# Kernel optimization log

Measured on AMD Instinct MI355X. Metric: run time of the kernel, lower is better.

Reference implementation:

```python
import jax, jax.numpy as jnp
import numpy as np

HIDDEN = 768
NUM_HEADS = 12
HEAD_DIM = HIDDEN // NUM_HEADS
WINDOW = 128
NEG = -1e30  # stand-in for -inf that is safe under autodiff


def setup_inputs() -> dict:
    key = jax.random.key(0)
    ks = jax.random.split(key, 12)
    B, S = 2, 2048
    hidden = jax.random.normal(ks[0], (B, S, HIDDEN), dtype=jnp.float32)
    attention_mask = jnp.ones((B, S), dtype=jnp.int32)
    global_mask = jax.random.randint(ks[1], (B, S), 0, 2, dtype=jnp.int32)
    def lin(kw, kb):
        W = jax.random.normal(kw, (HIDDEN, HIDDEN), dtype=jnp.float32) * 0.02
        b = jax.random.normal(kb, (HIDDEN,), dtype=jnp.float32) * 0.02
        return W, b
    Wq, bq = lin(ks[2], ks[3])
    Wk, bk = lin(ks[4], ks[5])
    Wv, bv = lin(ks[6], ks[7])
    Wo, bo = lin(ks[8], ks[9])
    return {"hidden": hidden, "attention_mask": attention_mask, "global_mask": global_mask,
            "Wq": Wq, "bq": bq, "Wk": Wk, "bk": bk, "Wv": Wv, "bv": bv, "Wo": Wo, "bo": bo}


def _attend(hidden, attention_mask, global_mask, Wq, bq, Wk, bk, Wv, bv, Wo, bo):
    B, S, H = hidden.shape
    def proj(W, b):
        # (B,S,H) -> (B,nh,S,hd); nn.Linear computes x @ W.T + b
        return (hidden @ W.T + b).reshape(B, S, NUM_HEADS, HEAD_DIM).transpose(0, 2, 1, 3)
    q, k, v = proj(Wq, bq), proj(Wk, bk), proj(Wv, bv)
    scale = jnp.asarray(np.sqrt(HEAD_DIM), dtype=hidden.dtype)
    scores = jnp.einsum('bhqd,bhkd->bhqk', q, k) / scale  # (B,nh,S,S)
    # sliding window mask: |i-j| <= WINDOW
    idx = jnp.arange(S)
    window = (jnp.abs(idx[:, None] - idx[None, :]) <= WINDOW)  # (S,S)
    g = global_mask.astype(bool)
    combined = window[None] | g[:, :, None] | g[:, None, :]     # (B,S,S)
    combined = combined & attention_mask.astype(bool)[:, None, :]  # pad mask on keys
    scores = jnp.where(combined[:, None, :, :], scores, NEG)
    attn = jax.nn.softmax(scores, axis=-1)
    # torch code zeroes NaN rows (fully masked); replicate safely
    attn = jnp.where(jnp.isnan(attn), 0.0, attn)
    out = jnp.einsum('bhqk,bhkd->bhqd', attn, v)  # (B,nh,S,hd)
    out = out.transpose(0, 2, 1, 3).reshape(B, S, H)
    return out @ Wo.T + bo


def reference(hidden, attention_mask, global_mask, Wq, bq, Wk, bk, Wv, bv, Wo, bo):
    return _attend(hidden, attention_mask, global_mask, Wq, bq, Wk, bk, Wv, bv, Wo, bo)
```

## Files before the change

### kernel.cpp

```cpp
#include <hip/hip_runtime.h>
#include <math.h>

#define S_LEN 2048
#define HID   768
#define NH    12
#define HD    64
#define WIN   128
#define NEGV  (-1e30f)
#define QSCALE 0.1803368801111204f

typedef __attribute__((ext_vector_type(8))) short short8v;
typedef __attribute__((ext_vector_type(4))) float float4v;
typedef unsigned short u16;

__device__ __forceinline__ u16 f2bf(float f) {
    union { float f; unsigned int u; } c; c.f = f;
    unsigned int u = c.u + 0x7FFFu + ((c.u >> 16) & 1u);
    return (u16)(u >> 16);
}

__device__ __forceinline__ short8v cvt8(float4 a, float4 b) {
    short8v t;
    t[0]=(short)f2bf(a.x); t[1]=(short)f2bf(a.y); t[2]=(short)f2bf(a.z); t[3]=(short)f2bf(a.w);
    t[4]=(short)f2bf(b.x); t[5]=(short)f2bf(b.y); t[6]=(short)f2bf(b.z); t[7]=(short)f2bf(b.w);
    return t;
}

__device__ __forceinline__ unsigned int pk2bf(float a, float b) {
    unsigned int r;
    asm("v_cvt_pk_bf16_f32 %0, %1, %2" : "=v"(r) : "v"(a), "v"(b));
    return r;
}

__device__ __forceinline__ float exp2_fast(float x) {
    float r;
    asm("v_exp_f32 %0, %1" : "=v"(r) : "v"(x));
    return r;
}

__device__ __forceinline__ void gload_lds16(const void* g, void* l) {
    __builtin_amdgcn_global_load_lds(
        (const __attribute__((address_space(1))) unsigned int*)g,
        (__attribute__((address_space(3))) unsigned int*)l, 16, 0, 0);
}

__global__ __launch_bounds__(256) void convert_inputs(
    const float* __restrict__ hidden, const float* __restrict__ Wq,
    const float* __restrict__ Wk, const float* __restrict__ Wv,
    const float* __restrict__ Wo, u16* __restrict__ hbf, u16* __restrict__ w4)
{
    const int y = blockIdx.y;
    const float* src; u16* dst; int n; float scale = 1.f;
    if (y == 0) { src = hidden; dst = hbf; n = 4096*HID; }
    else {
        src = (y==1) ? Wq : (y==2) ? Wk : (y==3) ? Wv : Wo;
        dst = w4 + (size_t)(y-1)*HID*HID;
        n = HID*HID;
        if (y == 1) scale = QSCALE;
    }
    const int idx = (blockIdx.x*256 + threadIdx.x) * 8;
    if (idx >= n) return;
    float4 f0 = *(const float4*)(src + idx);
    float4 f1 = *(const float4*)(src + idx + 4);
    f0.x*=scale; f0.y*=scale; f0.z*=scale; f0.w*=scale;
    f1.x*=scale; f1.y*=scale; f1.z*=scale; f1.w*=scale;
    *(short8v*)(dst + idx) = cvt8(f0, f1);
}

__global__ __launch_bounds__(256) void gemm_mfma(
    const u16* __restrict__ A, const u16* __restrict__ W4,
    const float* __restrict__ bA, const float* __restrict__ bB,
    const float* __restrict__ bC, u16* __restrict__ obf,
    u16* __restrict__ ovt, float* __restrict__ of32, int mode)
{
    __shared__ __align__(16) u16 As[128*32];
    __shared__ __align__(16) u16 Bs[128*32];

    const int tid = threadIdx.x;
    const int w = tid >> 6, l = tid & 63;
    const int lx = l & 15, lg = l >> 4;
    const int wr = w >> 1, wc = w & 1;
    const int m0 = blockIdx.x * 128, n0 = blockIdx.y * 128;
    const int z = (mode == 0) ? blockIdx.z : 3;
    const float* bias = (mode == 1) ? bA : (z == 0 ? bA : (z == 1 ? bB : bC));
    const float bscale = (mode == 0 && z == 0) ? QSCALE : 1.0f;
    const u16* Wp = W4 + (size_t)z * (HID*HID);

    float4v acc[4][4];
    const float4v fz = {0.f,0.f,0.f,0.f};
    #pragma unroll
    for (int i = 0; i < 4; i++)
        #pragma unroll
        for (int j = 0; j < 4; j++) acc[i][j] = fz;

    for (int kt = 0; kt < HID/32; kt++) {
        const int k0 = kt * 32;
        __syncthreads();
        #pragma unroll
        for (int rnd = 0; rnd < 2; rnd++) {
            const int ch  = rnd*256 + w*64 + l;
            const int row = ch >> 2, kc = ch & 3;
            gload_lds16(A  + (size_t)(m0+row)*HID + k0 + kc*8,
                        As + (size_t)(rnd*256 + w*64)*8);
            gload_lds16(Wp + (size_t)(n0+row)*HID + k0 + kc*8,
                        Bs + (size_t)(rnd*256 + w*64)*8);
        }
        __syncthreads();
        short8v af[4], bfr[4];
        #pragma unroll
        for (int i = 0; i < 4; i++) {
            af[i]  = *(const short8v*)(As + (wr*64 + i*16 + lx)*32 + lg*8);
            bfr[i] = *(const short8v*)(Bs + (wc*64 + i*16 + lx)*32 + lg*8);
        }
        #pragma unroll
        for (int i = 0; i < 4; i++)
            #pragma unroll
            for (int j = 0; j < 4; j++)
                acc[i][j] = __builtin_amdgcn_mfma_f32_16x16x32_bf16(af[i], bfr[j], acc[i][j], 0, 0, 0);
    }

    #pragma unroll
    for (int j = 0; j < 4; j++) {
        const int col = n0 + wc*64 + j*16 + lx;
        const float bval = bias[col] * bscale;
        const int hh = col >> 6, d = col & 63;
        #pragma unroll
        for (int i = 0; i < 4; i++) {
            const int rbase = m0 + wr*64 + i*16 + lg*4;
            const int bb = rbase >> 11, s = rbase & 2047;
            const float v0 = acc[i][j][0] + bval;
            const float v1 = acc[i][j][1] + bval;
            const float v2 = acc[i][j][2] + bval;
            const float v3 = acc[i][j][3] + bval;
            if (mode == 1) {
                of32[(size_t)(rbase+0)*HID + col] = v0;
                of32[(size_t)(rbase+1)*HID + col] = v1;
                of32[(size_t)(rbase+2)*HID + col] = v2;
                of32[(size_t)(rbase+3)*HID + col] = v3;
            } else if (z == 2) {
                uint2 ow; ow.x = pk2bf(v0, v1); ow.y = pk2bf(v2, v3);
                *(uint2*)&ovt[(((size_t)bb*NH + hh)*HD + d)*S_LEN + s] = ow;
            } else {
                u16* base = obf + (size_t)z * ((size_t)2*S_LEN*HID);
                base[(((size_t)bb*NH + hh)*S_LEN + s+0)*HD + d] = f2bf(v0);
                base[(((size_t)bb*NH + hh)*S_LEN + s+1)*HD + d] = f2bf(v1);
                base[(((size_t)bb*NH + hh)*S_LEN + s+2)*HD + d] = f2bf(v2);
                base[(((size_t)bb*NH + hh)*S_LEN + s+3)*HD + d] = f2bf(v3);
            }
        }
    }
}

__global__ __launch_bounds__(256) void attn_mfma(
    const u16* __restrict__ Q, const u16* __restrict__ K,
    const u16* __restrict__ Vt, const int* __restrict__ amask,
    const int* __restrict__ gmask, u16* __restrict__ AO)
{
    __shared__ __align__(16) u16 KsA[64*64], VsA[64*64];
    __shared__ __align__(16) u16 KsB[64*64], VsB[64*64];
    __shared__ __align__(16) u16 Ps[4*16*64];
    __shared__ __align__(16) float fAa[64], fBa[64];
    __shared__ __align__(16) float fAb[64], fBb[64];

    const int tid = threadIdx.x;
    const int w  = tid >> 6;
    const int l  = tid & 63;
    const int lx = l & 15;
    const int lg = l >> 4;

    const int bid = blockIdx.x;
    const int swz = (bid & 7) * 96 + (bid >> 3);
    const int q0 = (swz & 31) * 64;
    const int hb = swz >> 5;
    const int h  = hb % NH;
    const int b  = hb / NH;
    const size_t bh = ((size_t)b*NH + h) * S_LEN;

    const int q_glob = q0 + w*16 + lx;

    short8v aq[2];
    {
        const u16* qp = Q + (bh + q_glob)*HD + lg*8;
        aq[0] = *(const short8v*)(qp);
        aq[1] = *(const short8v*)(qp + 32);
    }
    const int gq = gmask[(size_t)b*S_LEN + q_glob];
    const float* fPa = gq ? fAa : fBa;
    const float* fPb = gq ? fAb : fBb;

    float m_i = NEGV, l_i = 0.f;
    float4v o_acc[4];
    const float4v fzv = {0.f, 0.f, 0.f, 0.f};
    #pragma unroll
    for (int db = 0; db < 4; db++) o_acc[db] = fzv;

    const int str = tid >> 2;
    const int stc = tid & 3;
    const int rb  = str * 128;
    const int sw  = (str & 7) << 4;
    const u16* Kbase = K + bh * HD;
    const u16* Vbase = Vt + (size_t)(b*NH + h) * HD * S_LEN;
    const int psw = (lx & 7) << 4;

    uint4 rk0, rk1, rv0, rv1;
    int ram = 0, rgk = 0;

#define STAGE_REGS(KT) do {                                                   \
    const int kk0_ = (KT) * 64;                                               \
    const u16* kp_ = Kbase + (size_t)(kk0_ + str)*HD + stc*16;                \
    rk0 = *(const uint4*)(kp_); rk1 = *(const uint4*)(kp_ + 8);               \
    const u16* vp_ = Vbase + (size_t)str*S_LEN + kk0_ + stc*16;               \
    rv0 = *(const uint4*)(vp_); rv1 = *(const uint4*)(vp_ + 8);               \
    if (tid < 64) {                                                           \
        ram = amask[(size_t)b*S_LEN + kk0_ + tid];                            \
        rgk = gmask[(size_t)b*S_LEN + kk0_ + tid];                            \
    }                                                                         \
} while(0)

#define WRITE_LDS(KS, VS, FA, FB) do {                                        \
    *(uint4*)((char*)(KS) + rb + ((stc*32)      ^ sw)) = rk0;                 \
    *(uint4*)((char*)(KS) + rb + ((stc*32 + 16) ^ sw)) = rk1;                 \
    *(uint4*)((char*)(VS) + rb + ((stc*32)      ^ sw)) = rv0;                 \
    *(uint4*)((char*)(VS) + rb + ((stc*32 + 16) ^ sw)) = rv1;                 \
    if (tid < 64) {                                                           \
        (FA)[tid] = ram ? 0.f : NEGV;                                         \
        (FB)[tid] = (ram && rgk) ? 0.f : NEGV;                                \
    }                                                                         \
} while(0)

#define COMPUTE(KS, VS, FA, FB, FP, K0) do {                                  \
                           \
    float4v sacc[4];                                                          \
    const int adq_ = ((K0) > q0) ? ((K0) - q0) : (q0 - (K0));                 \
    if (adq_ <= 64) {                                                         \
        _Pragma("unroll")                                                     \
        for (int kb = 0; kb < 4; kb++) {                                      \
            float4 fa4 = *(const float4*)&(FA)[kb*16 + lg*4];                 \
            sacc[kb][0]=fa4.x; sacc[kb][1]=fa4.y;                             \
            sacc[kb][2]=fa4.z; sacc[kb][3]=fa4.w;                             \
        }                                                                     \
    } else if (adq_ >= 192) {                                                 \
        _Pragma("unroll")                                                     \
        for (int kb = 0; kb < 4; kb++) {                                      \
            float4 fp4 = *(const float4*)&(FP)[kb*16 + lg*4];                 \
            sacc[kb][0]=fp4.x; sacc[kb][1]=fp4.y;                             \
            sacc[kb][2]=fp4.z; sacc[kb][3]=fp4.w;                             \
        }                                                                     \
    } else {                                                                  \
        _Pragma("unroll")                                                     \
        for (int kb = 0; kb < 4; kb++) {                                      \
            float4 fa4 = *(const float4*)&(FA)[kb*16 + lg*4];                 \
            float4 fb4 = *(const float4*)&(FB)[kb*16 + lg*4];                 \
            const int e_ = q_glob - ((K0) + kb*16 + lg*4);                    \
            _Pragma("unroll")                                                 \
            for (int r = 0; r < 4; r++) {                                     \
                int dd_ = e_ - r; dd_ = dd_ < 0 ? -dd_ : dd_;                 \
                const bool wing_ = (dd_ <= WIN) || gq;                        \
                sacc[kb][r] = wing_ ? (&fa4.x)[r] : (&fb4.x)[r];              \
            }                                                                 \
        }                                                                     \
    }                                                                         \
    __builtin_amdgcn_s_setprio(1);                                            \
    _Pragma("unroll")                                                         \
    for (int kb = 0; kb < 4; kb++) {                                          \
        const int key_ = kb*16 + lx;                                          \
        const int ksw_ = (key_ & 7) << 4;                                     \
        _Pragma("unroll")                                                     \
        for (int ks = 0; ks < 2; ks++) {                                      \
            short8v bk_ = *(const short8v*)((char*)(KS) + key_*128 +          \
                                            ((16*lg + 64*ks) ^ ksw_));        \
            sacc[kb] = __builtin_amdgcn_mfma_f32_16x16x32_bf16(bk_, aq[ks],   \
                                                          sacc[kb], 0, 0, 0); \
        }                                                                     \
    }                                                                         \
    __builtin_amdgcn_s_setprio(0);                                            \
                                \
    float mloc;                                                               \
    {                                                                         \
        float t0 = fmaxf(fmaxf(sacc[0][0], sacc[0][1]), sacc[0][2]);          \
        float t1 = fmaxf(fmaxf(sacc[0][3], sacc[1][0]), sacc[1][1]);          \
        float t2 = fmaxf(fmaxf(sacc[1][2], sacc[1][3]), sacc[2][0]);          \
        float t3 = fmaxf(fmaxf(sacc[2][1], sacc[2][2]), sacc[2][3]);          \
        float t4 = fmaxf(fmaxf(sacc[3][0], sacc[3][1]), sacc[3][2]);          \
        mloc = fmaxf(fmaxf(fmaxf(t0, t1), t2),                                \
                     fmaxf(fmaxf(t3, t4), sacc[3][3]));                       \
    }                                                                         \
    mloc = fmaxf(mloc, __shfl_xor(mloc, 16));                                 \
    mloc = fmaxf(mloc, __shfl_xor(mloc, 32));                                 \
    if (__any(mloc > m_i + 8.0f)) {                                           \
        const float mnew_ = fmaxf(m_i, mloc);                                 \
        const float sc_ = exp2_fast(m_i - mnew_);                             \
        l_i *= sc_;                                                           \
        _Pragma("unroll")                                                     \
        for (int db = 0; db < 4; db++)                                        \
            _Pragma("unroll")                                                 \
            for (int r = 0; r < 4; r++) o_acc[db][r] *= sc_;                  \
        m_i = mnew_;                                                          \
    }                                                                         \
    float p[4][4];                                                            \
    _Pragma("unroll")                                                         \
    for (int kb = 0; kb < 4; kb++)                                            \
        _Pragma("unroll")                                                     \
        for (int r = 0; r < 4; r++)                                           \
            p[kb][r] = exp2_fast(sacc[kb][r] - m_i);                          \
    {                                                                         \
        float s0 = (p[0][0]+p[0][1]) + (p[0][2]+p[0][3]);                     \
        float s1 = (p[1][0]+p[1][1]) + (p[1][2]+p[1][3]);                     \
        float s2 = (p[2][0]+p[2][1]) + (p[2][2]+p[2][3]);                     \
        float s3 = (p[3][0]+p[3][1]) + (p[3][2]+p[3][3]);                     \
        float lsum = (s0+s1) + (s2+s3);                                       \
        lsum += __shfl_xor(lsum, 16);                                         \
        lsum += __shfl_xor(lsum, 32);                                         \
        l_i += lsum;                                                          \
    }                                                                         \
    _Pragma("unroll")                                                         \
    for (int kb = 0; kb < 4; kb++) {                                          \
        uint2 pw;                                                             \
        pw.x = pk2bf(p[kb][0], p[kb][1]);                                     \
        pw.y = pk2bf(p[kb][2], p[kb][3]);                                     \
        *(uint2*)((char*)Ps + w*2048 + lx*128 + ((kb*32 + lg*8) ^ psw)) = pw; \
    }                                                                         \
    __builtin_amdgcn_s_setprio(1);                                            \
    _Pragma("unroll")                                                         \
    for (int ks = 0; ks < 2; ks++) {                                          \
        short8v pa_ = *(const short8v*)((char*)Ps + w*2048 + lx*128 +         \
                                        ((16*lg + 64*ks) ^ psw));             \
        _Pragma("unroll")                                                     \
        for (int db = 0; db < 4; db++) {                                      \
            const int drow_ = db*16 + lx;                                     \
            short8v bv_ = *(const short8v*)((char*)(VS) + drow_*128 +         \
                                    ((16*lg + 64*ks) ^ ((drow_ & 7) << 4)));  \
            o_acc[db] = __builtin_amdgcn_mfma_f32_16x16x32_bf16(bv_, pa_,     \
                                                          o_acc[db], 0, 0, 0);\
        }                                                                     \
    }                                                                         \
    __builtin_amdgcn_s_setprio(0);                                            \
} while(0)

    STAGE_REGS(0);
    WRITE_LDS(KsA, VsA, fAa, fBa);
    __syncthreads();

    for (int kt = 0; kt < S_LEN/64; kt += 2) {
        STAGE_REGS(kt+1);
        COMPUTE(KsA, VsA, fAa, fBa, fPa, kt*64);
        WRITE_LDS(KsB, VsB, fAb, fBb);
        __syncthreads();
        {
            const int kn = (kt+2 < S_LEN/64) ? (kt+2) : (S_LEN/64 - 1);
            STAGE_REGS(kn);
        }
        COMPUTE(KsB, VsB, fAb, fBb, fPb, (kt+1)*64);
        WRITE_LDS(KsA, VsA, fAa, fBa);
        __syncthreads();
    }

#undef STAGE_REGS
#undef WRITE_LDS
#undef COMPUTE

    {
        const float inv = 1.f / l_i;
        u16* op = AO + ((size_t)b*S_LEN + q_glob)*HID + h*HD + lg*4;
        #pragma unroll
        for (int db = 0; db < 4; db++) {
            uint2 ow;
            ow.x = pk2bf(o_acc[db][0]*inv, o_acc[db][1]*inv);
            ow.y = pk2bf(o_acc[db][2]*inv, o_acc[db][3]*inv);
            *(uint2*)(op + db*16) = ow;
        }
    }
}

extern "C" void kernel_launch(void* const* d_in, const int* in_sizes, int n_in,
                              void* d_out, int out_size, void* d_ws, size_t ws_size,
                              hipStream_t stream)
{
    const float* hidden = (const float*)d_in[0];
    const int*   amask  = (const int*)d_in[1];
    const int*   gmask  = (const int*)d_in[2];
    const float* Wq = (const float*)d_in[3];
    const float* bq = (const float*)d_in[4];
    const float* Wk = (const float*)d_in[5];
    const float* bk = (const float*)d_in[6];
    const float* Wv = (const float*)d_in[7];
    const float* bv = (const float*)d_in[8];
    const float* Wo = (const float*)d_in[9];
    const float* bo = (const float*)d_in[10];
    float* out = (float*)d_out;

    char* ws = (char*)d_ws;
    const size_t NTOK = (size_t)2 * S_LEN * HID;
    u16* hbf   = (u16*)(ws);
    u16* w4    = (u16*)(ws + 6291456);
    u16* qkvbf = (u16*)(ws + 11010048);
    u16* vtbf  = (u16*)(ws + 29884416);
    u16* aobf  = (u16*)(ws + 36175872);

    convert_inputs<<<dim3(1536, 5), 256, 0, stream>>>(hidden, Wq, Wk, Wv, Wo, hbf, w4);

    gemm_mfma<<<dim3(32, 6, 3), 256, 0, stream>>>(hbf, w4, bq, bk, bv, qkvbf, vtbf, nullptr, 0);

    u16* Qbf = qkvbf;
    u16* Kbf = qkvbf + NTOK;

    attn_mfma<<<dim3(768), 256, 0, stream>>>(Qbf, Kbf, vtbf, amask, gmask, aobf);

    gemm_mfma<<<dim3(32, 6), 256, 0, stream>>>(aobf, w4, bo, nullptr, nullptr, nullptr, nullptr, out, 1);
}
```

Measured before the change: 106.1 us.

## Split attention keys across two blocks and merge partial softmax results

The attention kernel now processes each query tile in two blocks, each covering half of the key range. Each block writes an unnormalized partial output plus its running max and sum, and a new merge kernel combines the two halves. This doubles the grid to raise occupancy and parallelism. K rows are permuted when staged into shared memory so the P fragment can be fed to the PV MFMA straight from registers, which removes the Ps LDS round-trip. The cost is an extra kernel launch and extra global traffic for the partials, plus losing the double-buffered K/V staging (now single buffer with two barriers per tile). Workspace regions that are no longer live (hidden bf16, the Wq part of the weights, Vt) are reused for the partials and the merged output.

```diff
diff --git a/kernel.cpp b/kernel.cpp
--- a/kernel.cpp
+++ b/kernel.cpp
@@ -8,6 +8,7 @@
 #define WIN   128
 #define NEGV  (-1e30f)
 #define QSCALE 0.1803368801111204f
+#define NROW  49152
 
 typedef __attribute__((ext_vector_type(8))) short short8v;
 typedef __attribute__((ext_vector_type(4))) float float4v;
@@ -36,6 +37,15 @@
     float r;
     asm("v_exp_f32 %0, %1" : "=v"(r) : "v"(x));
     return r;
+}
+
+__device__ __forceinline__ short8v mk8(unsigned a, unsigned b, unsigned c, unsigned d) {
+    union { short8v v; unsigned u[4]; } t;
+    t.u[0]=a; t.u[1]=b; t.u[2]=c; t.u[3]=d; return t.v;
+}
+
+__device__ __forceinline__ float bf2f(u16 v) {
+    union { float f; unsigned u; } c; c.u = ((unsigned)v) << 16; return c.f;
 }
 
 __device__ __forceinline__ void gload_lds16(const void* g, void* l) {
@@ -151,16 +161,16 @@
     }
 }
 
-__global__ __launch_bounds__(256) void attn_mfma(
+__global__ __launch_bounds__(256) void attn_split(
     const u16* __restrict__ Q, const u16* __restrict__ K,
     const u16* __restrict__ Vt, const int* __restrict__ amask,
-    const int* __restrict__ gmask, u16* __restrict__ AO)
+    const int* __restrict__ gmask, u16* __restrict__ O0,
+    u16* __restrict__ O1, float* __restrict__ Mp, float* __restrict__ Lp)
 {
-    __shared__ __align__(16) u16 KsA[64*64], VsA[64*64];
-    __shared__ __align__(16) u16 KsB[64*64], VsB[64*64];
-    __shared__ __align__(16) u16 Ps[4*16*64];
-    __shared__ __align__(16) float fAa[64], fBa[64];
-    __shared__ __align__(16) float fAb[64], fBb[64];
+    __shared__ __align__(16) u16 Ks[64*64];
+    __shared__ __align__(16) u16 Vs[64*64];
+    __shared__ __align__(16) float fA[64];
+    __shared__ __align__(16) float fB[64];
 
     const int tid = threadIdx.x;
     const int w  = tid >> 6;
@@ -169,9 +179,10 @@
     const int lg = l >> 4;
 
     const int bid = blockIdx.x;
-    const int swz = (bid & 7) * 96 + (bid >> 3);
-    const int q0 = (swz & 31) * 64;
-    const int hb = swz >> 5;
+    const int swz = (bid & 7) * 192 + (bid >> 3);
+    const int half = swz & 1;
+    const int q0 = ((swz >> 1) & 31) * 64;
+    const int hb = swz >> 6;
     const int h  = hb % NH;
     const int b  = hb / NH;
     const size_t bh = ((size_t)b*NH + h) * S_LEN;
@@ -185,8 +196,7 @@
         aq[1] = *(const short8v*)(qp + 32);
     }
     const int gq = gmask[(size_t)b*S_LEN + q_glob];
-    const float* fPa = gq ? fAa : fBa;
-    const float* fPb = gq ? fAb : fBb;
+    const float* fP = gq ? fA : fB;
 
     float m_i = NEGV, l_i = 0.f;
     float4v o_acc[4];
@@ -196,11 +206,14 @@
 
     const int str = tid >> 2;
     const int stc = tid & 3;
-    const int rb  = str * 128;
-    const int sw  = (str & 7) << 4;
+    const int xr  = (str & 32) | (((str>>2)&1)<<4) | (((str>>4)&1)<<3)
+                  | (((str>>3)&1)<<2) | (str & 3);
+    const int rbK = xr * 128;
+    const int swK = (xr & 7) << 4;
+    const int rbV = str * 128;
+    const int swV = (str & 7) << 4;
     const u16* Kbase = K + bh * HD;
     const u16* Vbase = Vt + (size_t)(b*NH + h) * HD * S_LEN;
-    const int psw = (lx & 7) << 4;
 
     uint4 rk0, rk1, rv0, rv1;
     int ram = 0, rgk = 0;
@@ -217,41 +230,44 @@
     }                                                                         \
 } while(0)
 
-#define WRITE_LDS(KS, VS, FA, FB) do {                                        \
-    *(uint4*)((char*)(KS) + rb + ((stc*32)      ^ sw)) = rk0;                 \
-    *(uint4*)((char*)(KS) + rb + ((stc*32 + 16) ^ sw)) = rk1;                 \
-    *(uint4*)((char*)(VS) + rb + ((stc*32)      ^ sw)) = rv0;                 \
-    *(uint4*)((char*)(VS) + rb + ((stc*32 + 16) ^ sw)) = rv1;                 \
+#define WRITE_LDS() do {                                                      \
+    *(uint4*)((char*)Ks + rbK + ((stc*32)      ^ swK)) = rk0;                 \
+    *(uint4*)((char*)Ks + rbK + ((stc*32 + 16) ^ swK)) = rk1;                 \
+    *(uint4*)((char*)Vs + rbV + ((stc*32)      ^ swV)) = rv0;                 \
+    *(uint4*)((char*)Vs + rbV + ((stc*32 + 16) ^ swV)) = rv1;                 \
     if (tid < 64) {                                                           \
-        (FA)[tid] = ram ? 0.f : NEGV;                                         \
-        (FB)[tid] = (ram && rgk) ? 0.f : NEGV;                                \
+        fA[tid] = ram ? 0.f : NEGV;                                           \
+        fB[tid] = (ram && rgk) ? 0.f : NEGV;                                  \
     }                                                                         \
 } while(0)
 
-#define COMPUTE(KS, VS, FA, FB, FP, K0) do {                                  \
-                           \
+#define COMPUTE(K0) do {                                                      \
+       \
     float4v sacc[4];                                                          \
     const int adq_ = ((K0) > q0) ? ((K0) - q0) : (q0 - (K0));                 \
     if (adq_ <= 64) {                                                         \
         _Pragma("unroll")                                                     \
         for (int kb = 0; kb < 4; kb++) {                                      \
-            float4 fa4 = *(const float4*)&(FA)[kb*16 + lg*4];                 \
+            const int base_ = 32*(kb>>1) + 8*lg + 4*(kb&1);                   \
+            float4 fa4 = *(const float4*)&fA[base_];                          \
             sacc[kb][0]=fa4.x; sacc[kb][1]=fa4.y;                             \
             sacc[kb][2]=fa4.z; sacc[kb][3]=fa4.w;                             \
         }                                                                     \
     } else if (adq_ >= 192) {                                                 \
         _Pragma("unroll")                                                     \
         for (int kb = 0; kb < 4; kb++) {                                      \
-            float4 fp4 = *(const float4*)&(FP)[kb*16 + lg*4];                 \
+            const int base_ = 32*(kb>>1) + 8*lg + 4*(kb&1);                   \
+            float4 fp4 = *(const float4*)&fP[base_];                          \
             sacc[kb][0]=fp4.x; sacc[kb][1]=fp4.y;                             \
             sacc[kb][2]=fp4.z; sacc[kb][3]=fp4.w;                             \
         }                                                                     \
     } else {                                                                  \
         _Pragma("unroll")                                                     \
         for (int kb = 0; kb < 4; kb++) {                                      \
-            float4 fa4 = *(const float4*)&(FA)[kb*16 + lg*4];                 \
-            float4 fb4 = *(const float4*)&(FB)[kb*16 + lg*4];                 \
-            const int e_ = q_glob - ((K0) + kb*16 + lg*4);                    \
+            const int base_ = 32*(kb>>1) + 8*lg + 4*(kb&1);                   \
+            float4 fa4 = *(const float4*)&fA[base_];                          \
+            float4 fb4 = *(const float4*)&fB[base_];                          \
+            const int e_ = q_glob - ((K0) + base_);                           \
             _Pragma("unroll")                                                 \
             for (int r = 0; r < 4; r++) {                                     \
                 int dd_ = e_ - r; dd_ = dd_ < 0 ? -dd_ : dd_;                 \
@@ -263,18 +279,17 @@
     __builtin_amdgcn_s_setprio(1);                                            \
     _Pragma("unroll")                                                         \
     for (int kb = 0; kb < 4; kb++) {                                          \
-        const int key_ = kb*16 + lx;                                          \
-        const int ksw_ = (key_ & 7) << 4;                                     \
+        const int row_ = kb*16 + lx;                                          \
+        const int ksw_ = (row_ & 7) << 4;                                     \
         _Pragma("unroll")                                                     \
         for (int ks = 0; ks < 2; ks++) {                                      \
-            short8v bk_ = *(const short8v*)((char*)(KS) + key_*128 +          \
+            short8v bk_ = *(const short8v*)((char*)Ks + row_*128 +            \
                                             ((16*lg + 64*ks) ^ ksw_));        \
             sacc[kb] = __builtin_amdgcn_mfma_f32_16x16x32_bf16(bk_, aq[ks],   \
                                                           sacc[kb], 0, 0, 0); \
         }                                                                     \
     }                                                                         \
     __builtin_amdgcn_s_setprio(0);                                            \
-                                \
     float mloc;                                                               \
     {                                                                         \
         float t0 = fmaxf(fmaxf(sacc[0][0], sacc[0][1]), sacc[0][2]);          \
@@ -313,23 +328,19 @@
         lsum += __shfl_xor(lsum, 32);                                         \
         l_i += lsum;                                                          \
     }                                                                         \
-    _Pragma("unroll")                                                         \
-    for (int kb = 0; kb < 4; kb++) {                                          \
-        uint2 pw;                                                             \
-        pw.x = pk2bf(p[kb][0], p[kb][1]);                                     \
-        pw.y = pk2bf(p[kb][2], p[kb][3]);                                     \
-        *(uint2*)((char*)Ps + w*2048 + lx*128 + ((kb*32 + lg*8) ^ psw)) = pw; \
-    }                                                                         \
+      \
     __builtin_amdgcn_s_setprio(1);                                            \
     _Pragma("unroll")                                                         \
-    for (int ks = 0; ks < 2; ks++) {                                          \
-        short8v pa_ = *(const short8v*)((char*)Ps + w*2048 + lx*128 +         \
-                                        ((16*lg + 64*ks) ^ psw));             \
+    for (int hh = 0; hh < 2; hh++) {                                          \
+        short8v pa_ = mk8(pk2bf(p[2*hh][0],   p[2*hh][1]),                    \
+                          pk2bf(p[2*hh][2],   p[2*hh][3]),                    \
+                          pk2bf(p[2*hh+1][0], p[2*hh+1][1]),                  \
+                          pk2bf(p[2*hh+1][2], p[2*hh+1][3]));                 \
         _Pragma("unroll")                                                     \
         for (int db = 0; db < 4; db++) {                                      \
             const int drow_ = db*16 + lx;                                     \
-            short8v bv_ = *(const short8v*)((char*)(VS) + drow_*128 +         \
-                                    ((16*lg + 64*ks) ^ ((drow_ & 7) << 4)));  \
+            short8v bv_ = *(const short8v*)((char*)Vs + drow_*128 +           \
+                                    ((16*lg + 64*hh) ^ ((drow_ & 7) << 4)));  \
             o_acc[db] = __builtin_amdgcn_mfma_f32_16x16x32_bf16(bv_, pa_,     \
                                                           o_acc[db], 0, 0, 0);\
         }                                                                     \
@@ -337,21 +348,17 @@
     __builtin_amdgcn_s_setprio(0);                                            \
 } while(0)
 
-    STAGE_REGS(0);
-    WRITE_LDS(KsA, VsA, fAa, fBa);
+    const int t0 = half * 16, t1 = t0 + 16;
+    STAGE_REGS(t0);
+    WRITE_LDS();
     __syncthreads();
 
-    for (int kt = 0; kt < S_LEN/64; kt += 2) {
-        STAGE_REGS(kt+1);
-        COMPUTE(KsA, VsA, fAa, fBa, fPa, kt*64);
-        WRITE_LDS(KsB, VsB, fAb, fBb);
+    for (int kt = t0; kt < t1; kt++) {
+        const int kn = (kt+1 < t1) ? (kt+1) : kt;
+        STAGE_REGS(kn);
+        COMPUTE(kt*64);
         __syncthreads();
-        {
-            const int kn = (kt+2 < S_LEN/64) ? (kt+2) : (S_LEN/64 - 1);
-            STAGE_REGS(kn);
-        }
-        COMPUTE(KsB, VsB, fAb, fBb, fPb, (kt+1)*64);
-        WRITE_LDS(KsA, VsA, fAa, fBa);
+        WRITE_LDS();
         __syncthreads();
     }
 
@@ -360,16 +367,56 @@
 #undef COMPUTE
 
     {
-        const float inv = 1.f / l_i;
-        u16* op = AO + ((size_t)b*S_LEN + q_glob)*HID + h*HD + lg*4;
+        u16* op = (half ? O1 : O0) + (bh + q_glob)*HD + lg*4;
         #pragma unroll
         for (int db = 0; db < 4; db++) {
             uint2 ow;
-            ow.x = pk2bf(o_acc[db][0]*inv, o_acc[db][1]*inv);
-            ow.y = pk2bf(o_acc[db][2]*inv, o_acc[db][3]*inv);
+            ow.x = pk2bf(o_acc[db][0], o_acc[db][1]);
+            ow.y = pk2bf(o_acc[db][2], o_acc[db][3]);
             *(uint2*)(op + db*16) = ow;
         }
-    }
+        if (lg == 0) {
+            Mp[half*NROW + bh + q_glob] = m_i;
+            Lp[half*NROW + bh + q_glob] = l_i;
+        }
+    }
+}
+
+__global__ __launch_bounds__(256) void attn_merge(
+    const u16* __restrict__ O0, const u16* __restrict__ O1,
+    const float* __restrict__ Mp, const float* __restrict__ Lp,
+    u16* __restrict__ AO)
+{
+    const int idx8 = (blockIdx.x*256 + threadIdx.x) * 8;
+    const int b   = idx8 / (S_LEN*HID);
+    const int rem = idx8 - b*(S_LEN*HID);
+    const int s   = rem / HID;
+    const int hd  = rem - s*HID;
+    const int hh  = hd >> 6;
+    const int d0  = hd & 63;
+    const int row = (b*NH + hh)*S_LEN + s;
+
+    const float m0 = Mp[row], m1 = Mp[NROW + row];
+    const float l0 = Lp[row], l1 = Lp[NROW + row];
+    const float m  = fmaxf(m0, m1);
+    const float w0 = exp2_fast(m0 - m);
+    const float w1 = exp2_fast(m1 - m);
+    const float inv = 1.f / (l0*w0 + l1*w1);
+
+    const size_t ioff = (size_t)row*HD + d0;
+    uint4 a = *(const uint4*)(O0 + ioff);
+    uint4 c = *(const uint4*)(O1 + ioff);
+    const u16* ap = (const u16*)&a;
+    const u16* cp = (const u16*)&c;
+    unsigned ow[4];
+    #pragma unroll
+    for (int j = 0; j < 4; j++) {
+        float f0 = (bf2f(ap[2*j])*w0   + bf2f(cp[2*j])*w1)   * inv;
+        float f1 = (bf2f(ap[2*j+1])*w0 + bf2f(cp[2*j+1])*w1) * inv;
+        ow[j] = pk2bf(f0, f1);
+    }
+    uint4 o; o.x=ow[0]; o.y=ow[1]; o.z=ow[2]; o.w=ow[3];
+    *(uint4*)(AO + idx8) = o;
 }
 
 extern "C" void kernel_launch(void* const* d_in, const int* in_sizes, int n_in,
@@ -393,6 +440,8 @@
     const size_t NTOK = (size_t)2 * S_LEN * HID;
     u16* hbf   = (u16*)(ws);
     u16* w4    = (u16*)(ws + 6291456);
+    float* Mp  = (float*)(ws + 6291456);
+    float* Lp  = Mp + 2*NROW;
     u16* qkvbf = (u16*)(ws + 11010048);
     u16* vtbf  = (u16*)(ws + 29884416);
     u16* aobf  = (u16*)(ws + 36175872);
@@ -404,7 +453,10 @@
     u16* Qbf = qkvbf;
     u16* Kbf = qkvbf + NTOK;
 
-    attn_mfma<<<dim3(768), 256, 0, stream>>>(Qbf, Kbf, vtbf, amask, gmask, aobf);
-
-    gemm_mfma<<<dim3(32, 6), 256, 0, stream>>>(aobf, w4, bo, nullptr, nullptr, nullptr, nullptr, out, 1);
-}
+    attn_split<<<dim3(1536), 256, 0, stream>>>(Qbf, Kbf, vtbf, amask, gmask,
+                                               aobf, hbf, Mp, Lp);
+
+    attn_merge<<<dim3(1536), 256, 0, stream>>>(aobf, hbf, Mp, Lp, vtbf);
+
+    gemm_mfma<<<dim3(32, 6), 256, 0, stream>>>(vtbf, w4, bo, nullptr, nullptr, nullptr, nullptr, out, 1);
+}
```

New measurement: 112.5 us. 1.06x slower.
